# Optimization experiments

Measured on AMD Instinct MI355X. Metric: run time of the kernel, lower is better.

Reference implementation:

```python
import jax, jax.numpy as jnp
import numpy as np
import math

B, D = 32768, 64

def setup_inputs() -> dict:
    key = jax.random.key(0)
    k1, k2, k3 = jax.random.split(key, 3)
    x = jax.random.normal(k1, (B, D), dtype=jnp.float32)
    grad_H = jax.random.normal(k2, (B, D), dtype=jnp.float32)
    # kaiming-normal-like init: std = sqrt(2 / fan_in), fan_in = D+1
    weight = jax.random.normal(k3, (D + 1, D * D), dtype=jnp.float32) * np.float32(math.sqrt(2.0 / (D + 1)))
    return {"x": x, "grad_H": grad_H, "weight": weight}

def reference(x, grad_H, weight):
    b, d = x.shape
    x1 = jnp.concatenate([x, jnp.ones((b, 1), dtype=x.dtype)], axis=1)  # (B, D+1)
    M = (x1 @ weight).reshape(b, d, d)                                   # (B, D, D)
    R = jnp.einsum('bik,bjk->bij', M, M) / jnp.asarray(math.sqrt(d), x.dtype)  # M @ M^T
    return jnp.einsum('bd,bde->be', grad_H, R)                           # (B, D)
```

## Files before the change

### kernel.cpp

```cpp
#include <hip/hip_runtime.h>
#include <stdint.h>

typedef __bf16    bf16x8  __attribute__((ext_vector_type(8)));
typedef float     f32x16v __attribute__((ext_vector_type(16)));
typedef float     f32x4v  __attribute__((ext_vector_type(4)));
typedef uint32_t  u32x4v  __attribute__((ext_vector_type(4)));
typedef unsigned short u16;

__device__ __forceinline__ u16 f32_to_bf16_rne(float f) {
  uint32_t u = __builtin_bit_cast(uint32_t, f);
  return (u16)((u + 0x7fffu + ((u >> 16) & 1u)) >> 16);
}

__device__ __forceinline__ uint32_t cvt_pk2(float a, float b) {
  uint32_t r;
  asm("v_cvt_pk_bf16_f32 %0, %1, %2" : "=v"(r) : "v"(a), "v"(b));
  return r;
}

__device__ __forceinline__ f32x16v mfma16(u32x4v a, u32x4v b, f32x16v c) {
  return __builtin_amdgcn_mfma_f32_32x32x16_bf16(
      __builtin_bit_cast(bf16x8, a), __builtin_bit_cast(bf16x8, b), c, 0, 0, 0);
}

__global__ __launch_bounds__(256) void prep_w(const float* __restrict__ W,
                                              u16* __restrict__ w1f,
                                              u16* __restrict__ w2f) {
  __shared__ float Wl[4096];
  const int jj = blockIdx.x;
  const int t  = threadIdx.x;
  for (int idx = t; idx < 4096; idx += 256) Wl[idx] = W[jj * 4096 + idx];
  __syncthreads();
  for (int p = t; p < 512; p += 256) {
    const int c2 = p >> 6, l = p & 63;
    const int ct = c2 >> 2, s = c2 & 3;
    const int rowA = ct * 32 + (l & 31);
    const int k0   = s * 16 + (l >> 5) * 8;
    u16 v1[8], v2[8];
    #pragma unroll
    for (int e = 0; e < 8; ++e) {
      v2[e] = f32_to_bf16_rne(Wl[rowA * 64 + k0 + e]);
      v1[e] = f32_to_bf16_rne(Wl[(k0 + e) * 64 + rowA]);
    }
    u32x4v pk1, pk2;
    #pragma unroll
    for (int q = 0; q < 4; ++q) {
      pk1[q] = (uint32_t)v1[2*q] | ((uint32_t)v1[2*q+1] << 16);
      pk2[q] = (uint32_t)v2[2*q] | ((uint32_t)v2[2*q+1] << 16);
    }
    *reinterpret_cast<u32x4v*>(w1f + jj * 4096 + p * 8) = pk1;
    *reinterpret_cast<u32x4v*>(w2f + jj * 4096 + p * 8) = pk2;
  }
}

__global__ __launch_bounds__(256) void rquad_main(
    const float* __restrict__ x, const float* __restrict__ g,
    const u16* __restrict__ w1f, const u16* __restrict__ w2f,
    float* __restrict__ out) {
  __shared__ u16 stage[2][8 * 4096];
  __shared__ u16 x1b[128 * 66];

  const int t    = threadIdx.x;
  const int lane = t & 63;
  const int wv   = t >> 6;
  const int bl   = lane & 31;
  const int half = lane >> 5;
  const long base = (long)blockIdx.x * 128;
  const int  srow = wv * 32 + bl;

  for (int idx = t; idx < 128 * 64; idx += 256) {
    int s = idx >> 6, c = idx & 63;
    x1b[s * 66 + c] = f32_to_bf16_rne(x[(base + s) * 64 + c]);
  }
  if (t < 128) x1b[t * 66 + 64] = (u16)0x3F80;

  f32x4v ka[4], kb[4];
  #pragma unroll
  for (int s = 0; s < 4; ++s) {
    const float* gp = g + (base + srow) * 64 + s * 16 + half * 8;
    ka[s] = *reinterpret_cast<const f32x4v*>(gp);
    kb[s] = *reinterpret_cast<const f32x4v*>(gp + 4);
  }

  f32x16v acc0, acc1;

  auto stage_chunk = [&](const u16* __restrict__ Wsrc, int c, int buf) {
    const int j0 = c * 8;
    const int nj = (j0 + 8 <= 65) ? 8 : (65 - j0);
    const int nq = nj * 8;
    for (int q = wv; q < nq; q += 4) {
      const u16* src = Wsrc + (size_t)j0 * 4096 + q * 512 + lane * 8;
      __builtin_amdgcn_global_load_lds(
          (const __attribute__((address_space(1))) void*)src,
          (__attribute__((address_space(3))) void*)(&stage[buf][q * 512]),
          16, 0, 0);
    }
  };

  auto compute_j = [&](int jl, int buf, int jglob) {
    const u16* sb = &stage[buf][jl * 4096];
    u32x4v B0[4], B1[4];
    #pragma unroll
    for (int s = 0; s < 4; ++s) {
      B0[s] = *reinterpret_cast<const u32x4v*>(sb + s * 512 + lane * 8);
      B1[s] = *reinterpret_cast<const u32x4v*>(sb + 2048 + s * 512 + lane * 8);
    }
    const u16 xu = x1b[srow * 66 + jglob];
    const float xf = __builtin_bit_cast(float, (uint32_t)xu << 16);
    u32x4v av[4];
    #pragma unroll
    for (int s = 0; s < 4; ++s) {
      av[s][0] = cvt_pk2(xf * ka[s][0], xf * ka[s][1]);
      av[s][1] = cvt_pk2(xf * ka[s][2], xf * ka[s][3]);
      av[s][2] = cvt_pk2(xf * kb[s][0], xf * kb[s][1]);
      av[s][3] = cvt_pk2(xf * kb[s][2], xf * kb[s][3]);
    }
    #pragma unroll
    for (int s = 0; s < 4; ++s) {
      acc0 = mfma16(av[s], B0[s], acc0);
      acc1 = mfma16(av[s], B1[s], acc1);
    }
  };

  auto run_pass = [&](const u16* __restrict__ Wsrc) {
    #pragma unroll
    for (int r = 0; r < 16; ++r) { acc0[r] = 0.0f; acc1[r] = 0.0f; }
    stage_chunk(Wsrc, 0, 0);
    __syncthreads();
    for (int c = 0; c < 9; ++c) {
      if (c + 1 < 9) stage_chunk(Wsrc, c + 1, (c + 1) & 1);
      const int j0 = c * 8;
      if (j0 + 8 <= 65) {
        #pragma unroll
        for (int jl = 0; jl < 8; ++jl) compute_j(jl, c & 1, j0 + jl);
      } else {
        compute_j(0, c & 1, j0);
      }
      __syncthreads();
    }
  };

  __syncthreads();

  run_pass(w1f);

  {
    float* scr = reinterpret_cast<float*>(&stage[0][0]) + wv * (32 * 68);
    #pragma unroll
    for (int r = 0; r < 16; ++r) {
      const int rr = (r & 3) + 8 * (r >> 2) + 4 * half;
      scr[rr * 68 + bl]      = acc0[r];
      scr[rr * 68 + 32 + bl] = acc1[r];
    }
    #pragma unroll
    for (int s = 0; s < 4; ++s) {
      const float* vp = scr + bl * 68 + s * 16 + half * 8;
      ka[s] = *reinterpret_cast<const f32x4v*>(vp);
      kb[s] = *reinterpret_cast<const f32x4v*>(vp + 4);
    }
  }
  __syncthreads();

  run_pass(w2f);

  {
    float* ocr = reinterpret_cast<float*>(&stage[0][0]) + wv * (32 * 68);
    #pragma unroll
    for (int r = 0; r < 16; ++r) {
      const int rr = (r & 3) + 8 * (r >> 2) + 4 * half;
      ocr[rr * 68 + bl]      = acc0[r] * 0.125f;
      ocr[rr * 68 + 32 + bl] = acc1[r] * 0.125f;
    }
  }
  __syncthreads();
  for (int idx = t; idx < 2048; idx += 256) {
    const int b = idx >> 4, c4 = (idx & 15) * 4;
    const float* src = reinterpret_cast<const float*>(&stage[0][0]) +
                       (b >> 5) * (32 * 68) + (b & 31) * 68 + c4;
    f32x4v v4 = *reinterpret_cast<const f32x4v*>(src);
    *reinterpret_cast<f32x4v*>(out + (base + b) * 64 + c4) = v4;
  }
}

extern "C" void kernel_launch(void* const* d_in, const int* in_sizes, int n_in,
                              void* d_out, int out_size, void* d_ws, size_t ws_size,
                              hipStream_t stream) {
  const float* x = (const float*)d_in[0];
  const float* g = (const float*)d_in[1];
  const float* W = (const float*)d_in[2];
  float* o = (float*)d_out;
  u16* w1f = (u16*)d_ws;
  u16* w2f = w1f + 65 * 4096;
  hipLaunchKernelGGL(prep_w, dim3(65), dim3(256), 0, stream, W, w1f, w2f);
  hipLaunchKernelGGL(rquad_main, dim3(256), dim3(256), 0, stream, x, g, w1f, w2f, o);
}
```

Before: 55.63 us.

## Split the j-reduction across two wave groups and switch MFMA to fp16

Switches the main kernel from 256 to 512 threads. The 65-step reduction over j is split between two groups of four waves, each staging its own half of W into separate double buffers, and the two partial accumulators are summed through LDS at the end of each pass. Each wave now computes two 32-row tiles against one 32-column weight tile. A-operand scaling moves from f32 multiplies plus bf16 packing to packed fp16 multiplies, and weights and x are stored in fp16 for the fp16 MFMA. This doubles the waves per block to hide latency and removes conversion work, but adds cross-group LDS reductions and extra syncs, and fp16 range or precision could differ from bf16.

```diff
diff --git a/kernel.cpp b/kernel.cpp
--- a/kernel.cpp
+++ b/kernel.cpp
@@ -1,31 +1,22 @@
 #include <hip/hip_runtime.h>
 #include <stdint.h>
 
-typedef __bf16    bf16x8  __attribute__((ext_vector_type(8)));
+typedef _Float16  f16;
+typedef f16       f16x2  __attribute__((ext_vector_type(2)));
+typedef f16       f16x8  __attribute__((ext_vector_type(8)));
 typedef float     f32x16v __attribute__((ext_vector_type(16)));
 typedef float     f32x4v  __attribute__((ext_vector_type(4)));
 typedef uint32_t  u32x4v  __attribute__((ext_vector_type(4)));
 typedef unsigned short u16;
 
-__device__ __forceinline__ u16 f32_to_bf16_rne(float f) {
-  uint32_t u = __builtin_bit_cast(uint32_t, f);
-  return (u16)((u + 0x7fffu + ((u >> 16) & 1u)) >> 16);
-}
-
-__device__ __forceinline__ uint32_t cvt_pk2(float a, float b) {
-  uint32_t r;
-  asm("v_cvt_pk_bf16_f32 %0, %1, %2" : "=v"(r) : "v"(a), "v"(b));
-  return r;
-}
-
-__device__ __forceinline__ f32x16v mfma16(u32x4v a, u32x4v b, f32x16v c) {
-  return __builtin_amdgcn_mfma_f32_32x32x16_bf16(
-      __builtin_bit_cast(bf16x8, a), __builtin_bit_cast(bf16x8, b), c, 0, 0, 0);
+__device__ __forceinline__ f32x16v mfma16h(u32x4v a, u32x4v b, f32x16v c) {
+  return __builtin_amdgcn_mfma_f32_32x32x16_f16(
+      __builtin_bit_cast(f16x8, a), __builtin_bit_cast(f16x8, b), c, 0, 0, 0);
 }
 
 __global__ __launch_bounds__(256) void prep_w(const float* __restrict__ W,
-                                              u16* __restrict__ w1f,
-                                              u16* __restrict__ w2f) {
+                                              u16* __restrict__ w1h,
+                                              u16* __restrict__ w2h) {
   __shared__ float Wl[4096];
   const int jj = blockIdx.x;
   const int t  = threadIdx.x;
@@ -39,8 +30,8 @@
     u16 v1[8], v2[8];
     #pragma unroll
     for (int e = 0; e < 8; ++e) {
-      v2[e] = f32_to_bf16_rne(Wl[rowA * 64 + k0 + e]);
-      v1[e] = f32_to_bf16_rne(Wl[(k0 + e) * 64 + rowA]);
+      v2[e] = __builtin_bit_cast(u16, (f16)Wl[rowA * 64 + k0 + e]);
+      v1[e] = __builtin_bit_cast(u16, (f16)Wl[(k0 + e) * 64 + rowA]);
     }
     u32x4v pk1, pk2;
     #pragma unroll
@@ -48,48 +39,62 @@
       pk1[q] = (uint32_t)v1[2*q] | ((uint32_t)v1[2*q+1] << 16);
       pk2[q] = (uint32_t)v2[2*q] | ((uint32_t)v2[2*q+1] << 16);
     }
-    *reinterpret_cast<u32x4v*>(w1f + jj * 4096 + p * 8) = pk1;
-    *reinterpret_cast<u32x4v*>(w2f + jj * 4096 + p * 8) = pk2;
-  }
-}
-
-__global__ __launch_bounds__(256) void rquad_main(
+    *reinterpret_cast<u32x4v*>(w1h + jj * 4096 + p * 8) = pk1;
+    *reinterpret_cast<u32x4v*>(w2h + jj * 4096 + p * 8) = pk2;
+  }
+}
+
+__global__ __launch_bounds__(512, 2) void rquad_main(
     const float* __restrict__ x, const float* __restrict__ g,
-    const u16* __restrict__ w1f, const u16* __restrict__ w2f,
+    const u16* __restrict__ w1h, const u16* __restrict__ w2h,
     float* __restrict__ out) {
-  __shared__ u16 stage[2][8 * 4096];
+  __shared__ u16 stage[4][4 * 4096];
   __shared__ u16 x1b[128 * 66];
 
   const int t    = threadIdx.x;
   const int lane = t & 63;
   const int wv   = t >> 6;
+  const int jq   = wv >> 2;
+  const int p    = (wv >> 1) & 1;
+  const int ct   = wv & 1;
   const int bl   = lane & 31;
   const int half = lane >> 5;
   const long base = (long)blockIdx.x * 128;
-  const int  srow = wv * 32 + bl;
-
-  for (int idx = t; idx < 128 * 64; idx += 256) {
+  const int r0 = p * 64 + bl;
+  const int r1 = r0 + 32;
+
+  for (int idx = t; idx < 128 * 64; idx += 512) {
     int s = idx >> 6, c = idx & 63;
-    x1b[s * 66 + c] = f32_to_bf16_rne(x[(base + s) * 64 + c]);
-  }
-  if (t < 128) x1b[t * 66 + 64] = (u16)0x3F80;
-
-  f32x4v ka[4], kb[4];
+    x1b[s * 66 + c] = __builtin_bit_cast(u16, (f16)x[(base + s) * 64 + c]);
+  }
+  if (t < 128) x1b[t * 66 + 64] = (u16)0x3C00;
+
+  f16x2 z0[4][4], z1[4][4];
   #pragma unroll
   for (int s = 0; s < 4; ++s) {
-    const float* gp = g + (base + srow) * 64 + s * 16 + half * 8;
-    ka[s] = *reinterpret_cast<const f32x4v*>(gp);
-    kb[s] = *reinterpret_cast<const f32x4v*>(gp + 4);
+    const float* gp0 = g + (base + r0) * 64 + s * 16 + half * 8;
+    const float* gp1 = g + (base + r1) * 64 + s * 16 + half * 8;
+    f32x4v a = *reinterpret_cast<const f32x4v*>(gp0);
+    f32x4v b = *reinterpret_cast<const f32x4v*>(gp0 + 4);
+    f32x4v c = *reinterpret_cast<const f32x4v*>(gp1);
+    f32x4v d = *reinterpret_cast<const f32x4v*>(gp1 + 4);
+    z0[s][0] = f16x2{(f16)a[0], (f16)a[1]}; z0[s][1] = f16x2{(f16)a[2], (f16)a[3]};
+    z0[s][2] = f16x2{(f16)b[0], (f16)b[1]}; z0[s][3] = f16x2{(f16)b[2], (f16)b[3]};
+    z1[s][0] = f16x2{(f16)c[0], (f16)c[1]}; z1[s][1] = f16x2{(f16)c[2], (f16)c[3]};
+    z1[s][2] = f16x2{(f16)d[0], (f16)d[1]}; z1[s][3] = f16x2{(f16)d[2], (f16)d[3]};
   }
 
   f32x16v acc0, acc1;
 
-  auto stage_chunk = [&](const u16* __restrict__ Wsrc, int c, int buf) {
-    const int j0 = c * 8;
-    const int nj = (j0 + 8 <= 65) ? 8 : (65 - j0);
-    const int nq = nj * 8;
-    for (int q = wv; q < nq; q += 4) {
-      const u16* src = Wsrc + (size_t)j0 * 4096 + q * 512 + lane * 8;
+  auto stage_chunk = [&](const u16* __restrict__ Wsrc, int stream, int ci) {
+    if (ci > 8 || (stream == 1 && ci == 8)) return;
+    if (jq != stream) return;
+    const int j0 = (stream == 0) ? ci * 4 : 33 + ci * 4;
+    const int nq = (stream == 0 && ci == 8) ? 8 : 32;
+    const int buf = stream * 2 + (ci & 1);
+    const int w4 = wv & 3;
+    for (int q = w4; q < nq; q += 4) {
+      const u16* src = Wsrc + (size_t)(j0 + (q >> 3)) * 4096 + (q & 7) * 512 + lane * 8;
       __builtin_amdgcn_global_load_lds(
           (const __attribute__((address_space(1))) void*)src,
           (__attribute__((address_space(3))) void*)(&stage[buf][q * 512]),
@@ -97,28 +102,27 @@
     }
   };
 
-  auto compute_j = [&](int jl, int buf, int jglob) {
-    const u16* sb = &stage[buf][jl * 4096];
-    u32x4v B0[4], B1[4];
+  auto compute_j = [&](int buf, int jl, int jglob) {
+    const u16* sb = &stage[buf][jl * 4096 + ct * 2048];
+    u32x4v B[4];
+    #pragma unroll
+    for (int s = 0; s < 4; ++s)
+      B[s] = *reinterpret_cast<const u32x4v*>(sb + s * 512 + lane * 8);
+    const f16 xh0 = __builtin_bit_cast(f16, x1b[r0 * 66 + jglob]);
+    const f16 xh1 = __builtin_bit_cast(f16, x1b[r1 * 66 + jglob]);
+    const f16x2 xx0 = f16x2{xh0, xh0}, xx1 = f16x2{xh1, xh1};
     #pragma unroll
     for (int s = 0; s < 4; ++s) {
-      B0[s] = *reinterpret_cast<const u32x4v*>(sb + s * 512 + lane * 8);
-      B1[s] = *reinterpret_cast<const u32x4v*>(sb + 2048 + s * 512 + lane * 8);
-    }
-    const u16 xu = x1b[srow * 66 + jglob];
-    const float xf = __builtin_bit_cast(float, (uint32_t)xu << 16);
-    u32x4v av[4];
-    #pragma unroll
-    for (int s = 0; s < 4; ++s) {
-      av[s][0] = cvt_pk2(xf * ka[s][0], xf * ka[s][1]);
-      av[s][1] = cvt_pk2(xf * ka[s][2], xf * ka[s][3]);
-      av[s][2] = cvt_pk2(xf * kb[s][0], xf * kb[s][1]);
-      av[s][3] = cvt_pk2(xf * kb[s][2], xf * kb[s][3]);
-    }
-    #pragma unroll
-    for (int s = 0; s < 4; ++s) {
-      acc0 = mfma16(av[s], B0[s], acc0);
-      acc1 = mfma16(av[s], B1[s], acc1);
+      u32x4v a0, a1;
+      #pragma unroll
+      for (int q = 0; q < 4; ++q) {
+        f16x2 p0 = xx0 * z0[s][q];
+        f16x2 p1 = xx1 * z1[s][q];
+        a0[q] = __builtin_bit_cast(uint32_t, p0);
+        a1[q] = __builtin_bit_cast(uint32_t, p1);
+      }
+      acc0 = mfma16h(a0, B[s], acc0);
+      acc1 = mfma16h(a1, B[s], acc1);
     }
   };
 
@@ -126,15 +130,25 @@
     #pragma unroll
     for (int r = 0; r < 16; ++r) { acc0[r] = 0.0f; acc1[r] = 0.0f; }
     stage_chunk(Wsrc, 0, 0);
+    stage_chunk(Wsrc, 1, 0);
     __syncthreads();
-    for (int c = 0; c < 9; ++c) {
-      if (c + 1 < 9) stage_chunk(Wsrc, c + 1, (c + 1) & 1);
-      const int j0 = c * 8;
-      if (j0 + 8 <= 65) {
-        #pragma unroll
-        for (int jl = 0; jl < 8; ++jl) compute_j(jl, c & 1, j0 + jl);
+    for (int st = 0; st <= 8; ++st) {
+      stage_chunk(Wsrc, 0, st + 1);
+      stage_chunk(Wsrc, 1, st + 1);
+      if (jq == 0) {
+        const int buf = st & 1;
+        if (st < 8) {
+          #pragma unroll
+          for (int jl = 0; jl < 4; ++jl) compute_j(buf, jl, st * 4 + jl);
+        } else {
+          compute_j(buf, 0, 32);
+        }
       } else {
-        compute_j(0, c & 1, j0);
+        if (st < 8) {
+          const int buf = 2 + (st & 1);
+          #pragma unroll
+          for (int jl = 0; jl < 4; ++jl) compute_j(buf, jl, 33 + st * 4 + jl);
+        }
       }
       __syncthreads();
     }
@@ -142,43 +156,69 @@
 
   __syncthreads();
 
-  run_pass(w1f);
-
-  {
-    float* scr = reinterpret_cast<float*>(&stage[0][0]) + wv * (32 * 68);
-    #pragma unroll
-    for (int r = 0; r < 16; ++r) {
-      const int rr = (r & 3) + 8 * (r >> 2) + 4 * half;
-      scr[rr * 68 + bl]      = acc0[r];
-      scr[rr * 68 + 32 + bl] = acc1[r];
-    }
-    #pragma unroll
-    for (int s = 0; s < 4; ++s) {
-      const float* vp = scr + bl * 68 + s * 16 + half * 8;
-      ka[s] = *reinterpret_cast<const f32x4v*>(vp);
-      kb[s] = *reinterpret_cast<const f32x4v*>(vp + 4);
-    }
-  }
-  __syncthreads();
-
-  run_pass(w2f);
-
-  {
-    float* ocr = reinterpret_cast<float*>(&stage[0][0]) + wv * (32 * 68);
-    #pragma unroll
-    for (int r = 0; r < 16; ++r) {
-      const int rr = (r & 3) + 8 * (r >> 2) + 4 * half;
-      ocr[rr * 68 + bl]      = acc0[r] * 0.125f;
-      ocr[rr * 68 + 32 + bl] = acc1[r] * 0.125f;
-    }
-  }
-  __syncthreads();
-  for (int idx = t; idx < 2048; idx += 256) {
+  run_pass(w1h);
+
+  float* vl = reinterpret_cast<float*>(&stage[0][0]);
+  if (jq == 0) {
+    #pragma unroll
+    for (int r = 0; r < 16; ++r) {
+      const int rr = (r & 3) + 8 * (r >> 2) + 4 * half;
+      vl[(p * 64 + rr) * 68 + ct * 32 + bl]      = acc0[r];
+      vl[(p * 64 + 32 + rr) * 68 + ct * 32 + bl] = acc1[r];
+    }
+  }
+  __syncthreads();
+  if (jq == 1) {
+    #pragma unroll
+    for (int r = 0; r < 16; ++r) {
+      const int rr = (r & 3) + 8 * (r >> 2) + 4 * half;
+      vl[(p * 64 + rr) * 68 + ct * 32 + bl]      += acc0[r];
+      vl[(p * 64 + 32 + rr) * 68 + ct * 32 + bl] += acc1[r];
+    }
+  }
+  __syncthreads();
+  #pragma unroll
+  for (int s = 0; s < 4; ++s) {
+    const float* vp0 = &vl[r0 * 68 + s * 16 + half * 8];
+    const float* vp1 = &vl[r1 * 68 + s * 16 + half * 8];
+    f32x4v a = *reinterpret_cast<const f32x4v*>(vp0);
+    f32x4v b = *reinterpret_cast<const f32x4v*>(vp0 + 4);
+    f32x4v c = *reinterpret_cast<const f32x4v*>(vp1);
+    f32x4v d = *reinterpret_cast<const f32x4v*>(vp1 + 4);
+    z0[s][0] = f16x2{(f16)a[0], (f16)a[1]}; z0[s][1] = f16x2{(f16)a[2], (f16)a[3]};
+    z0[s][2] = f16x2{(f16)b[0], (f16)b[1]}; z0[s][3] = f16x2{(f16)b[2], (f16)b[3]};
+    z1[s][0] = f16x2{(f16)c[0], (f16)c[1]}; z1[s][1] = f16x2{(f16)c[2], (f16)c[3]};
+    z1[s][2] = f16x2{(f16)d[0], (f16)d[1]}; z1[s][3] = f16x2{(f16)d[2], (f16)d[3]};
+  }
+  __syncthreads();
+
+  run_pass(w2h);
+
+  if (jq == 0) {
+    #pragma unroll
+    for (int r = 0; r < 16; ++r) {
+      const int rr = (r & 3) + 8 * (r >> 2) + 4 * half;
+      vl[(p * 64 + rr) * 68 + ct * 32 + bl]      = acc0[r];
+      vl[(p * 64 + 32 + rr) * 68 + ct * 32 + bl] = acc1[r];
+    }
+  }
+  __syncthreads();
+  if (jq == 1) {
+    #pragma unroll
+    for (int r = 0; r < 16; ++r) {
+      const int rr = (r & 3) + 8 * (r >> 2) + 4 * half;
+      vl[(p * 64 + rr) * 68 + ct * 32 + bl]      += acc0[r];
+      vl[(p * 64 + 32 + rr) * 68 + ct * 32 + bl] += acc1[r];
+    }
+  }
+  __syncthreads();
+  for (int idx = t; idx < 2048; idx += 512) {
     const int b = idx >> 4, c4 = (idx & 15) * 4;
-    const float* src = reinterpret_cast<const float*>(&stage[0][0]) +
-                       (b >> 5) * (32 * 68) + (b & 31) * 68 + c4;
-    f32x4v v4 = *reinterpret_cast<const f32x4v*>(src);
-    *reinterpret_cast<f32x4v*>(out + (base + b) * 64 + c4) = v4;
+    f32x4v v4 = *reinterpret_cast<const f32x4v*>(&vl[b * 68 + c4]);
+    f32x4v o;
+    o[0] = v4[0] * 0.125f; o[1] = v4[1] * 0.125f;
+    o[2] = v4[2] * 0.125f; o[3] = v4[3] * 0.125f;
+    *reinterpret_cast<f32x4v*>(out + (base + b) * 64 + c4) = o;
   }
 }
 
@@ -189,8 +229,8 @@
   const float* g = (const float*)d_in[1];
   const float* W = (const float*)d_in[2];
   float* o = (float*)d_out;
-  u16* w1f = (u16*)d_ws;
-  u16* w2f = w1f + 65 * 4096;
-  hipLaunchKernelGGL(prep_w, dim3(65), dim3(256), 0, stream, W, w1f, w2f);
-  hipLaunchKernelGGL(rquad_main, dim3(256), dim3(256), 0, stream, x, g, w1f, w2f, o);
-}
+  u16* w1h = (u16*)d_ws;
+  u16* w2h = w1h + 65 * 4096;
+  hipLaunchKernelGGL(prep_w, dim3(65), dim3(256), 0, stream, W, w1h, w2h);
+  hipLaunchKernelGGL(rquad_main, dim3(256), dim3(512), 0, stream, x, g, w1h, w2h, o);
+}
```

New measurement: 52.97 us. -4.8%, faster.
